# Kernel tuning notes

Hardware: AMD Instinct MI355X
Metric: run time of the kernel (lower is better)

Reference implementation:

```python
import jax, jax.numpy as jnp
import numpy as np

TEMPERATURE = 1.0
WEIGHT = 1.0


def _transitivity_sum(rel):
    """rel: [N, N] relation probabilities for one (batch, relation) slice.
    Computes sum_{a,b,c} relu(rel[a,b] - rel[a,c] * rel[b,c]) via a scan over c
    (outer product of column c), keeping memory at O(N^2) instead of O(N^3)."""
    def step(acc, col):  # col = rel[:, c], shape [N]
        viol = jax.nn.relu(rel - col[:, None] * col[None, :])  # [N, N]
        return acc + jnp.sum(viol), None
    acc, _ = jax.lax.scan(step, jnp.zeros((), rel.dtype), rel.T)
    return acc


def setup_inputs() -> dict:
    key = jax.random.key(0)
    B, N, R = 2, 512, 4
    relation_logits = jax.random.normal(key, (B, N, N, R), dtype=jnp.float32)
    entity_masks = jnp.ones((B, N), dtype=jnp.int32)
    return {"relation_logits": relation_logits, "entity_masks": entity_masks}


def reference(relation_logits, entity_masks):
    B, N, _, R = relation_logits.shape
    probs = jax.nn.sigmoid(relation_logits / TEMPERATURE)  # [B, N, N, R]
    m = (entity_masks > 0).astype(probs.dtype)             # [B, N]
    rel = probs * m[:, :, None, None] * m[:, None, :, None]
    # flatten (batch, relation) and vmap the per-matrix cubic reduction
    rel_br = jnp.transpose(rel, (0, 3, 1, 2)).reshape(B * R, N, N)
    per = jax.vmap(_transitivity_sum)(rel_br)              # [B*R]
    # per-batch loss = sum_r / R; final = weight * mean over batch
    return WEIGHT * jnp.sum(per) / (R * B)
```

## Files before the change

### kernel.cpp

```cpp
#include <hip/hip_runtime.h>
#include <math.h>

#define N      512
#define RNUM   4
#define BNUM   2
#define NSLICE (RNUM * BNUM)
#define TILE   128
#define CT     64
#define LSTR   136
#define CSPLIT 8
#define NCOLB  16
#define SCALE  0.0625f

typedef _Float16 half2_t __attribute__((ext_vector_type(2)));

__device__ __forceinline__ unsigned int h2u(half2_t h) {
  return __builtin_bit_cast(unsigned int, h);
}
__device__ __forceinline__ half2_t u2h(unsigned int u) {
  return __builtin_bit_cast(half2_t, u);
}

#if __has_builtin(__builtin_amdgcn_fdot2)
__device__ __forceinline__ float fdot2_(half2_t a, half2_t b, float c) {
  return __builtin_amdgcn_fdot2(a, b, c, false);
}
#else
__device__ __forceinline__ float fdot2_(half2_t a, half2_t b, float c) {
  return c + (float)a.x * (float)b.x + (float)a.y * (float)b.y;
}
#endif

__device__ __forceinline__ float sigmoidf_(float x) {
  return 1.0f / (1.0f + __expf(-x));
}

__global__ void zero_out_kernel(float* out) { out[0] = 0.0f; }

__global__ __launch_bounds__(256) void prep_f16_kernel(const float* __restrict__ logits,
                                                       const int* __restrict__ masks,
                                                       _Float16* __restrict__ P,
                                                       float* __restrict__ out) {
  if (blockIdx.x == 0 && threadIdx.x == 0) out[0] = 0.0f;
  int t = blockIdx.x * 256 + threadIdx.x;
  int b = t >> 18;
  int rem = t & (N * N - 1);
  int i = rem >> 9;
  int j = rem & (N - 1);
  float4 lg = *(const float4*)(logits + (size_t)t * 4);
  float mm = ((masks[b * N + i] > 0) && (masks[b * N + j] > 0)) ? 1.0f : 0.0f;
  size_t base = (size_t)b * RNUM * N * N + rem;
  P[base + 0 * (size_t)N * N] = (_Float16)(mm * sigmoidf_(lg.x));
  P[base + 1 * (size_t)N * N] = (_Float16)(mm * sigmoidf_(lg.y));
  P[base + 2 * (size_t)N * N] = (_Float16)(mm * sigmoidf_(lg.z));
  P[base + 3 * (size_t)N * N] = (_Float16)(mm * sigmoidf_(lg.w));
}

__global__ __launch_bounds__(256, 4) void work_f16_kernel(const _Float16* __restrict__ P,
                                                          float* __restrict__ out) {
  __shared__ _Float16 tA[CT][LSTR];
  __shared__ _Float16 tB[CT][LSTR];
  __shared__ float wsum[4];

  const int tid = threadIdx.x;
  const int bid = blockIdx.x;

  if (bid < NCOLB) {
    const int s    = bid >> 1;
    const int half = bid & 1;
    const int c    = half * 256 + tid;
    const _Float16* col = P + (size_t)s * N * N + c;
    float sum = 0.0f;
#pragma unroll 16
    for (int a = 0; a < N; ++a) sum += (float)col[(size_t)a * N];
    float v = sum * ((float)N - sum);
    for (int off = 32; off > 0; off >>= 1) v += __shfl_down(v, off, 64);
    const int wid = tid >> 6;
    if ((tid & 63) == 0) wsum[wid] = v;
    __syncthreads();
    if (tid == 0)
      atomicAdd(out, (wsum[0] + wsum[1] + wsum[2] + wsum[3]) * SCALE);
    return;
  }

  const int m  = bid - NCOLB;
  const int bt = m & 3;
  const int at = (m >> 2) & 3;
  const int s  = (m >> 4) & 7;
  const int cz = m >> 7;
  const int a0 = at * TILE;
  const int b0 = bt * TILE;
  const int c0 = cz * CT;

  const int ta = tid & 15;
  const int tb = tid >> 4;

  const _Float16* Ph = P + (size_t)s * N * N;

  {
    const int u   = tid & 127;
    const int h   = tid >> 7;
    const int isB = u >> 6;
    const int p   = u & 63;
    const int r0  = (isB ? b0 : a0) + 2 * p;
    const int cc0 = c0 + h * 32;
    const _Float16* s0row = Ph + (size_t)r0 * N + cc0;
    const _Float16* s1row = s0row + N;
    _Float16* dst = isB ? &tB[h * 32][2 * p] : &tA[h * 32][2 * p];
    uint4 q0 = ((const uint4*)s0row)[0];
    uint4 q1 = ((const uint4*)s0row)[1];
    uint4 q2 = ((const uint4*)s0row)[2];
    uint4 q3 = ((const uint4*)s0row)[3];
    uint4 p0 = ((const uint4*)s1row)[0];
    uint4 p1 = ((const uint4*)s1row)[1];
    uint4 p2 = ((const uint4*)s1row)[2];
    uint4 p3 = ((const uint4*)s1row)[3];
    unsigned int w0[16] = {q0.x, q0.y, q0.z, q0.w, q1.x, q1.y, q1.z, q1.w,
                           q2.x, q2.y, q2.z, q2.w, q3.x, q3.y, q3.z, q3.w};
    unsigned int w1[16] = {p0.x, p0.y, p0.z, p0.w, p1.x, p1.y, p1.z, p1.w,
                           p2.x, p2.y, p2.z, p2.w, p3.x, p3.y, p3.z, p3.w};
#pragma unroll
    for (int k = 0; k < 16; ++k) {
      unsigned int lo = (w1[k] << 16) | (w0[k] & 0xFFFFu);
      unsigned int hi = (w1[k] & 0xFFFF0000u) | (w0[k] >> 16);
      *(unsigned int*)(dst + (size_t)(2 * k) * LSTR)     = lo;
      *(unsigned int*)(dst + (size_t)(2 * k + 1) * LSTR) = hi;
    }
  }

  half2_t rab2[8][4];
#pragma unroll
  for (int x = 0; x < 8; ++x) {
    int ga = a0 + ((x >> 2) << 6) + ta * 4 + (x & 3);
    uint2 u0 = *(const uint2*)(Ph + (size_t)ga * N + b0 + tb * 4);
    uint2 u1 = *(const uint2*)(Ph + (size_t)ga * N + b0 + 64 + tb * 4);
    rab2[x][0] = u2h(u0.x); rab2[x][1] = u2h(u0.y);
    rab2[x][2] = u2h(u1.x); rab2[x][3] = u2h(u1.y);
  }

  float acc[8];
#pragma unroll
  for (int x = 0; x < 8; ++x) acc[x] = 0.0f;

  const half2_t kOne = {(_Float16)1.0f, (_Float16)1.0f};

  __syncthreads();

#pragma unroll 4
  for (int c = 0; c < CT; ++c) {
    uint2 ua0 = *(const uint2*)&tA[c][ta * 4];
    uint2 ua1 = *(const uint2*)&tA[c][64 + ta * 4];
    uint2 ub0 = *(const uint2*)&tB[c][tb * 4];
    uint2 ub1 = *(const uint2*)&tB[c][64 + tb * 4];
    half2_t av[4] = {u2h(ua0.x), u2h(ua0.y), u2h(ua1.x), u2h(ua1.y)};
    half2_t bv[4] = {u2h(ub0.x), u2h(ub0.y), u2h(ub1.x), u2h(ub1.y)};
#pragma unroll
    for (int x = 0; x < 8; ++x) {
      _Float16 as = (x & 1) ? av[x >> 1].y : av[x >> 1].x;
      half2_t asp = {as, as};
      float a_ = acc[x];
#pragma unroll
      for (int yp = 0; yp < 4; ++yp) {
        half2_t t2 = rab2[x][yp] - asp * bv[yp];
        half2_t p2 = u2h(h2u(t2) & 0x7FFF7FFFu);
        a_ = fdot2_(p2, kOne, a_);
      }
      acc[x] = a_;
    }
  }

  float tsum = 0.0f;
#pragma unroll
  for (int x = 0; x < 8; ++x) tsum += acc[x];

  for (int off = 32; off > 0; off >>= 1) tsum += __shfl_down(tsum, off, 64);

  const int wid = tid >> 6;
  if ((tid & 63) == 0) wsum[wid] = tsum;
  __syncthreads();
  if (tid == 0)
    atomicAdd(out, (wsum[0] + wsum[1] + wsum[2] + wsum[3]) * SCALE);
}

#define FCT    64
#define FSTR   132
#define FCSPL  4

__global__ __launch_bounds__(256, 2) void work_f32_fallback(const float* __restrict__ logits,
                                                            const int* __restrict__ masks,
                                                            float* __restrict__ out) {
  __shared__ __align__(16) float tA[FCT][FSTR];
  __shared__ __align__(16) float tB[FCT][FSTR];
  __shared__ float wsum[4];

  const int tid = threadIdx.x;
  const int bid = blockIdx.x;

  if (bid < NCOLB) {
    const int s    = bid >> 1;
    const int half = bid & 1;
    const int c    = half * 256 + tid;
    const int bb   = s >> 2;
    const int r    = s & 3;
    const int* mrow = masks + bb * N;
    float mc = (mrow[c] > 0) ? 1.0f : 0.0f;
    float sum = 0.0f;
#pragma unroll 4
    for (int a = 0; a < N; ++a) {
      float ma = (mrow[a] > 0) ? 1.0f : 0.0f;
      size_t idx = ((size_t)(bb * N + a) * N + c) * RNUM + r;
      sum += sigmoidf_(logits[idx]) * ma * mc;
    }
    float v = sum * ((float)N - sum);
    for (int off = 32; off > 0; off >>= 1) v += __shfl_down(v, off, 64);
    const int wid = tid >> 6;
    if ((tid & 63) == 0) wsum[wid] = v;
    __syncthreads();
    if (tid == 0)
      atomicAdd(out, (wsum[0] + wsum[1] + wsum[2] + wsum[3]) * SCALE);
    return;
  }

  const int m  = bid - NCOLB;
  const int bt = m & 3;
  const int at = (m >> 2) & 3;
  const int s  = (m >> 4) & 7;
  const int cz = m >> 7;
  const int a0 = at * TILE;
  const int b0 = bt * TILE;
  const int bb = s >> 2;
  const int r  = s & 3;
  const int cbeg = cz * (N / FCSPL);
  const int cend = cbeg + (N / FCSPL);

  const int ta = tid & 15;
  const int tb = tid >> 4;
  const int* mrow = masks + bb * N;

  float rab[8][8];
#pragma unroll
  for (int x = 0; x < 8; ++x) {
    int ra = a0 + ((x >> 2) << 6) + ta * 4 + (x & 3);
    float ma = (mrow[ra] > 0) ? 1.0f : 0.0f;
#pragma unroll
    for (int y = 0; y < 8; ++y) {
      int cb = b0 + ((y >> 2) << 6) + tb * 4 + (y & 3);
      float mb = (mrow[cb] > 0) ? 1.0f : 0.0f;
      size_t idx = ((size_t)(bb * N + ra) * N + cb) * RNUM + r;
      rab[x][y] = sigmoidf_(logits[idx]) * ma * mb;
    }
  }

  float acc[8][2];
#pragma unroll
  for (int x = 0; x < 8; ++x) { acc[x][0] = 0.0f; acc[x][1] = 0.0f; }

  for (int c0 = cbeg; c0 < cend; c0 += FCT) {
    __syncthreads();
#pragma unroll
    for (int it = 0; it < 32; ++it) {
      int e = it * 256 + tid;
      int c = e & 63;
      int i = e >> 6;
      int pc = ((((i >> 2) ^ ((c >> 2) & 31)) & 31) << 2) | (i & 3);
      float mc = (mrow[c0 + c] > 0) ? 1.0f : 0.0f;
      {
        float mi = (mrow[a0 + i] > 0) ? 1.0f : 0.0f;
        size_t idx = ((size_t)(bb * N + a0 + i) * N + (c0 + c)) * RNUM + r;
        tA[c][pc] = sigmoidf_(logits[idx]) * mi * mc;
      }
      {
        float mi = (mrow[b0 + i] > 0) ? 1.0f : 0.0f;
        size_t idx = ((size_t)(bb * N + b0 + i) * N + (c0 + c)) * RNUM + r;
        tB[c][pc] = sigmoidf_(logits[idx]) * mi * mc;
      }
    }
    __syncthreads();

#pragma unroll 2
    for (int cg = 0; cg < FCT / 4; ++cg) {
      const float* pa = &tA[cg * 4][((ta ^ cg) & 31) << 2];
      const float* pb = &tB[cg * 4][((tb ^ cg) & 31) << 2];
#pragma unroll
      for (int dc = 0; dc < 4; ++dc) {
        float4 a0v = *(const float4*)(pa + dc * FSTR);
        float4 a1v = *(const float4*)(pa + dc * FSTR + 64);
        float4 b0v = *(const float4*)(pb + dc * FSTR);
        float4 b1v = *(const float4*)(pb + dc * FSTR + 64);
        float avv[8] = {a0v.x, a0v.y, a0v.z, a0v.w, a1v.x, a1v.y, a1v.z, a1v.w};
        float bvv[8] = {b0v.x, b0v.y, b0v.z, b0v.w, b1v.x, b1v.y, b1v.z, b1v.w};
#pragma unroll
        for (int x = 0; x < 8; ++x) {
#pragma unroll
          for (int y = 0; y < 4; ++y)
            acc[x][0] += fabsf(fmaf(-avv[x], bvv[y], rab[x][y]));
#pragma unroll
          for (int y = 4; y < 8; ++y)
            acc[x][1] += fabsf(fmaf(-avv[x], bvv[y], rab[x][y]));
        }
      }
    }
  }

  float tsum = 0.0f;
#pragma unroll
  for (int x = 0; x < 8; ++x) tsum += acc[x][0] + acc[x][1];
  for (int off = 32; off > 0; off >>= 1) tsum += __shfl_down(tsum, off, 64);
  const int wid = tid >> 6;
  if ((tid & 63) == 0) wsum[wid] = tsum;
  __syncthreads();
  if (tid == 0)
    atomicAdd(out, (wsum[0] + wsum[1] + wsum[2] + wsum[3]) * SCALE);
}

extern "C" void kernel_launch(void* const* d_in, const int* in_sizes, int n_in,
                              void* d_out, int out_size, void* d_ws, size_t ws_size,
                              hipStream_t stream) {
  const float* logits = (const float*)d_in[0];
  const int*   masks  = (const int*)d_in[1];
  float*       out    = (float*)d_out;

  const size_t P_BYTES = (size_t)NSLICE * N * N * sizeof(_Float16);

  if (ws_size >= P_BYTES) {
    _Float16* P = (_Float16*)d_ws;
    prep_f16_kernel<<<(BNUM * N * N) / 256, 256, 0, stream>>>(logits, masks, P, out);
    const int nblocks = NCOLB + 4 * 4 * NSLICE * CSPLIT;
    work_f16_kernel<<<nblocks, 256, 0, stream>>>(P, out);
  } else {
    zero_out_kernel<<<1, 1, 0, stream>>>(out);
    const int nblocks = NCOLB + 4 * 4 * NSLICE * FCSPL;
    work_f32_fallback<<<nblocks, 256, 0, stream>>>(logits, masks, out);
  }
}
```

Before: 117.3 us.

## Halve c-chunk per block, double c-split, and use contiguous 8-wide thread tiles

Shrinks the per-block c chunk from 64 to 32 and doubles the c-split count, so twice as many blocks each do half the c work. Shared-memory tiles shrink, and launch bounds rise to 8 blocks per multiprocessor for higher occupancy. Each thread's 8x8 (a,b) micro-tile becomes contiguous, so loads use single 16-byte accesses instead of paired 8-byte ones. The cost is that each block loads its rab register tile for only 32 c steps, so that load is amortised over less compute, and the higher launch bound may cause register spilling.

```diff
diff --git a/kernel.cpp b/kernel.cpp
--- a/kernel.cpp
+++ b/kernel.cpp
@@ -6,9 +6,9 @@
 #define BNUM   2
 #define NSLICE (RNUM * BNUM)
 #define TILE   128
-#define CT     64
+#define CT     32
 #define LSTR   136
-#define CSPLIT 8
+#define CSPLIT 16
 #define NCOLB  16
 #define SCALE  0.0625f
 
@@ -56,10 +56,10 @@
   P[base + 3 * (size_t)N * N] = (_Float16)(mm * sigmoidf_(lg.w));
 }
 
-__global__ __launch_bounds__(256, 4) void work_f16_kernel(const _Float16* __restrict__ P,
+__global__ __launch_bounds__(256, 8) void work_f16_kernel(const _Float16* __restrict__ P,
                                                           float* __restrict__ out) {
-  __shared__ _Float16 tA[CT][LSTR];
-  __shared__ _Float16 tB[CT][LSTR];
+  __shared__ __align__(16) _Float16 tA[CT][LSTR];
+  __shared__ __align__(16) _Float16 tB[CT][LSTR];
   __shared__ float wsum[4];
 
   const int tid = threadIdx.x;
@@ -103,24 +103,18 @@
     const int isB = u >> 6;
     const int p   = u & 63;
     const int r0  = (isB ? b0 : a0) + 2 * p;
-    const int cc0 = c0 + h * 32;
+    const int cc0 = c0 + h * 16;
     const _Float16* s0row = Ph + (size_t)r0 * N + cc0;
     const _Float16* s1row = s0row + N;
-    _Float16* dst = isB ? &tB[h * 32][2 * p] : &tA[h * 32][2 * p];
+    _Float16* dst = isB ? &tB[h * 16][2 * p] : &tA[h * 16][2 * p];
     uint4 q0 = ((const uint4*)s0row)[0];
     uint4 q1 = ((const uint4*)s0row)[1];
-    uint4 q2 = ((const uint4*)s0row)[2];
-    uint4 q3 = ((const uint4*)s0row)[3];
-    uint4 p0 = ((const uint4*)s1row)[0];
-    uint4 p1 = ((const uint4*)s1row)[1];
-    uint4 p2 = ((const uint4*)s1row)[2];
-    uint4 p3 = ((const uint4*)s1row)[3];
-    unsigned int w0[16] = {q0.x, q0.y, q0.z, q0.w, q1.x, q1.y, q1.z, q1.w,
-                           q2.x, q2.y, q2.z, q2.w, q3.x, q3.y, q3.z, q3.w};
-    unsigned int w1[16] = {p0.x, p0.y, p0.z, p0.w, p1.x, p1.y, p1.z, p1.w,
-                           p2.x, p2.y, p2.z, p2.w, p3.x, p3.y, p3.z, p3.w};
-#pragma unroll
-    for (int k = 0; k < 16; ++k) {
+    uint4 r0v = ((const uint4*)s1row)[0];
+    uint4 r1v = ((const uint4*)s1row)[1];
+    unsigned int w0[8] = {q0.x, q0.y, q0.z, q0.w, q1.x, q1.y, q1.z, q1.w};
+    unsigned int w1[8] = {r0v.x, r0v.y, r0v.z, r0v.w, r1v.x, r1v.y, r1v.z, r1v.w};
+#pragma unroll
+    for (int k = 0; k < 8; ++k) {
       unsigned int lo = (w1[k] << 16) | (w0[k] & 0xFFFFu);
       unsigned int hi = (w1[k] & 0xFFFF0000u) | (w0[k] >> 16);
       *(unsigned int*)(dst + (size_t)(2 * k) * LSTR)     = lo;
@@ -131,11 +125,10 @@
   half2_t rab2[8][4];
 #pragma unroll
   for (int x = 0; x < 8; ++x) {
-    int ga = a0 + ((x >> 2) << 6) + ta * 4 + (x & 3);
-    uint2 u0 = *(const uint2*)(Ph + (size_t)ga * N + b0 + tb * 4);
-    uint2 u1 = *(const uint2*)(Ph + (size_t)ga * N + b0 + 64 + tb * 4);
-    rab2[x][0] = u2h(u0.x); rab2[x][1] = u2h(u0.y);
-    rab2[x][2] = u2h(u1.x); rab2[x][3] = u2h(u1.y);
+    int ga = a0 + ta * 8 + x;
+    uint4 q = *(const uint4*)(Ph + (size_t)ga * N + b0 + tb * 8);
+    rab2[x][0] = u2h(q.x); rab2[x][1] = u2h(q.y);
+    rab2[x][2] = u2h(q.z); rab2[x][3] = u2h(q.w);
   }
 
   float acc[8];
@@ -148,12 +141,10 @@
 
 #pragma unroll 4
   for (int c = 0; c < CT; ++c) {
-    uint2 ua0 = *(const uint2*)&tA[c][ta * 4];
-    uint2 ua1 = *(const uint2*)&tA[c][64 + ta * 4];
-    uint2 ub0 = *(const uint2*)&tB[c][tb * 4];
-    uint2 ub1 = *(const uint2*)&tB[c][64 + tb * 4];
-    half2_t av[4] = {u2h(ua0.x), u2h(ua0.y), u2h(ua1.x), u2h(ua1.y)};
-    half2_t bv[4] = {u2h(ub0.x), u2h(ub0.y), u2h(ub1.x), u2h(ub1.y)};
+    uint4 ua = *(const uint4*)&tA[c][ta * 8];
+    uint4 ub = *(const uint4*)&tB[c][tb * 8];
+    half2_t av[4] = {u2h(ua.x), u2h(ua.y), u2h(ua.z), u2h(ua.w)};
+    half2_t bv[4] = {u2h(ub.x), u2h(ub.y), u2h(ub.z), u2h(ub.w)};
 #pragma unroll
     for (int x = 0; x < 8; ++x) {
       _Float16 as = (x & 1) ? av[x >> 1].y : av[x >> 1].x;
```

Measured after the change: 114.3 us. 2.6% less time.
